# Kernel optimization log

Hardware: AMD Instinct MI355X
Metric: run time of the kernel (lower is better)

## Reference

```python
import jax, jax.numpy as jnp
import numpy as np

# Dims and constants
B, DIN, H = 32768, 256, 256
STEPS = 3                 # ode_steps (>1 -> RK2 branch)
DT = 1.0 / STEPS
TAU_MIN = 0.2
ALPHA = 0.1               # plastic (hebb) mixing coefficient
ETA = 0.1                 # hebb learning rate
DECAY = 0.99              # hebb trace decay
MOE_WEIGHT = 1.0


def setup_inputs() -> dict:
    key = jax.random.key(0)
    ks = jax.random.split(key, 8)
    s = 0.02
    return {
        "x": jax.random.normal(ks[0], (B, DIN), dtype=jnp.float32),
        "h": jax.random.normal(ks[1], (B, H), dtype=jnp.float32),
        "hebb_ih": jnp.zeros((DIN, H), dtype=jnp.float32),
        "hebb_hh": jnp.zeros((H, H), dtype=jnp.float32),
        # PlasticSynapse base weights (torch Linear layout [out, in])
        "W_ih": jax.random.normal(ks[2], (H, DIN), dtype=jnp.float32) * s,
        "b_ih": jnp.zeros((H,), dtype=jnp.float32),
        "W_hh": jax.random.normal(ks[3], (H, H), dtype=jnp.float32) * s,
        "b_hh": jnp.zeros((H,), dtype=jnp.float32),
        # tau_net: Linear(DIN+H -> H) -> SiLU -> Linear(H -> H) -> Softplus
        "W_t1": jax.random.normal(ks[4], (H, DIN + H), dtype=jnp.float32) * s,
        "b_t1": jnp.zeros((H,), dtype=jnp.float32),
        "W_t2": jax.random.normal(ks[5], (H, H), dtype=jnp.float32) * s,
        "b_t2": jnp.zeros((H,), dtype=jnp.float32),
    }


def reference(x, h, hebb_ih, hebb_hh, W_ih, b_ih, W_hh, b_hh, W_t1, b_t1, W_t2, b_t2):
    bsz = x.shape[0]
    step_moe = MOE_WEIGHT / STEPS

    def syn(inp, W, b, hebb):
        # PlasticSynapse: fixed weight + alpha-scaled Hebbian trace
        return inp @ (W.T + ALPHA * hebb) + b

    def tau_net(hh):
        z = jnp.concatenate([x, hh], axis=-1)          # [B, DIN+H]
        u = z @ W_t1.T + b_t1
        u = u * jax.nn.sigmoid(u)                      # SiLU
        return jax.nn.softplus(u @ W_t2.T + b_t2) + TAU_MIN

    def dynamics(hh, heb_ih, heb_hh):
        interaction = jnp.tanh(syn(x, W_ih, b_ih, heb_ih) + syn(hh, W_hh, b_hh, heb_hh))
        return (-hh + interaction) / tau_net(hh)

    def update_hebb(hebb, pre, post):
        # decayed trace + batch-mean outer product, scaled by per-step moe weight
        return DECAY * hebb + (ETA * step_moe / bsz) * (pre.T @ post)

    # RK2 loop (steps = 3, fixed) with mid-point Hebbian updates, per original forward
    for _ in range(STEPS):
        k1 = dynamics(h, hebb_ih, hebb_hh)
        h_mid = h + 0.5 * DT * k1
        hebb_ih = update_hebb(hebb_ih, x, h_mid)
        hebb_hh = update_hebb(hebb_hh, h_mid, h_mid)
        k2 = dynamics(h_mid, hebb_ih, hebb_hh)
        h = h + DT * k2
    return h
```

## Files before the change

### kernel.cpp

```cpp
#include <hip/hip_runtime.h>
#include <stdint.h>

typedef unsigned short u16;
typedef short v8s __attribute__((ext_vector_type(8)));
typedef short v4s __attribute__((ext_vector_type(4)));
typedef float v4f __attribute__((ext_vector_type(4)));

#define NB 32768
#define ND 256
#define DTF (1.0f/3.0f)
#define ALPHA 0.1f
#define DECAY 0.99f
#define TAU_MIN 0.2f
#define HEBB_SCALE (0.1f*(1.0f/3.0f)/32768.0f)

__device__ __forceinline__ float b2f(u16 h){ return __uint_as_float(((unsigned)h)<<16); }
__device__ __forceinline__ u16 f2b(float f){
  unsigned u = __float_as_uint(f);
  u += 0x7FFFu + ((u>>16)&1u);
  return (u16)(u>>16);
}

__device__ __forceinline__ void async16(const void* g, void* l){
  __builtin_amdgcn_global_load_lds((const __attribute__((address_space(1))) unsigned*)g,
                                   (__attribute__((address_space(3))) unsigned*)l, 16, 0, 0);
}

__device__ __forceinline__ void waitv(int n){
  switch(n){
    case 9: asm volatile("s_waitcnt vmcnt(9)" ::: "memory"); break;
    case 8: asm volatile("s_waitcnt vmcnt(8)" ::: "memory"); break;
    case 7: asm volatile("s_waitcnt vmcnt(7)" ::: "memory"); break;
    case 6: asm volatile("s_waitcnt vmcnt(6)" ::: "memory"); break;
    case 4: asm volatile("s_waitcnt vmcnt(4)" ::: "memory"); break;
    case 2: asm volatile("s_waitcnt vmcnt(2)" ::: "memory"); break;
    default: asm volatile("s_waitcnt vmcnt(0)" ::: "memory"); break;
  }
}

__global__ void k_copy(const float* __restrict__ x, const float* __restrict__ h,
                       u16* __restrict__ x_bf, u16* __restrict__ h_bf,
                       float* __restrict__ h_state){
  const long tot = (long)NB*ND/4;
  for (long i = blockIdx.x*(long)blockDim.x + threadIdx.x; i < tot;
       i += (long)gridDim.x*blockDim.x){
    v4f xv = *(const v4f*)(x + 4*i);
    v4f hv = *(const v4f*)(h + 4*i);
    u16 t4[4], t5[4];
#pragma unroll
    for (int e=0;e<4;++e){ t4[e] = f2b(xv[e]); t5[e] = f2b(hv[e]); }
    *(v4s*)(x_bf + 4*i) = *(v4s*)t4;
    *(v4s*)(h_bf + 4*i) = *(v4s*)t5;
    *(v4f*)(h_state + 4*i) = hv;
  }
}

__global__ void k_transpose_x(const float* __restrict__ x, u16* __restrict__ xT){
  __shared__ u16 ld[64*65];
  int bt = blockIdx.x >> 2, it = blockIdx.x & 3;
  long b0 = (long)bt*64; int i0 = it*64;
  int t = threadIdx.x;
#pragma unroll
  for (int e=0;e<16;++e){
    int idx = e*256 + t; int r = idx>>6, c = idx&63;
    ld[c + r*65] = f2b(x[(b0+r)*ND + i0 + c]);
  }
  __syncthreads();
#pragma unroll
  for (int e=0;e<16;++e){
    int idx = e*256 + t; int rr = idx>>6, cc = idx&63;
    xT[(long)(i0+rr)*NB + b0 + cc] = ld[cc*65 + rr];
  }
}

__global__ void k_prep_w(const float* __restrict__ W_ih, const float* __restrict__ W_hh,
                         const float* __restrict__ W_t1, const float* __restrict__ W_t2,
                         const float* __restrict__ hebb_ih, const float* __restrict__ hebb_hh,
                         u16* __restrict__ weff_ih, u16* __restrict__ weff_hh,
                         u16* __restrict__ wt1a, u16* __restrict__ wt1b, u16* __restrict__ wt2){
  int i = blockIdx.x*blockDim.x + threadIdx.x;
  if (i >= ND*ND) return;
  int n = i >> 8, k = i & 255;
  weff_ih[i] = f2b(W_ih[i] + ALPHA*hebb_ih[k*ND + n]);
  weff_hh[i] = f2b(W_hh[i] + ALPHA*hebb_hh[k*ND + n]);
  wt1a[i] = f2b(W_t1[n*512 + k]);
  wt1b[i] = f2b(W_t1[n*512 + 256 + k]);
  wt2[i]  = f2b(W_t2[i]);
}

__launch_bounds__(512,2)
__global__ void k_gemmP(const u16* __restrict__ x_bf, const u16* __restrict__ wt1a,
                        const float* __restrict__ b_t1, u16* __restrict__ P){
  __shared__ u16 lA[128*40];
  __shared__ u16 lB[256*40];
  int t = threadIdx.x, lid = t&63, wid = t>>6, wm = wid>>2, wn = wid&3, lr = lid&15, lg = lid>>4;
  long row0 = (long)blockIdx.x*128;
  v4f z = {0.f,0.f,0.f,0.f};
  v4f acc[4][4];
#pragma unroll
  for (int a=0;a<4;++a)
#pragma unroll
    for (int b=0;b<4;++b) acc[a][b] = z;
  for (int c=0; c<8; ++c){
    __syncthreads();
    { int r=t>>2, sg=t&3;
      *(v8s*)&lA[r*40+sg*8] = *(const v8s*)(x_bf + (row0+r)*ND + c*32 + sg*8); }
#pragma unroll
    for (int it2=0; it2<2; ++it2){
      int s2=t+it2*512; int n=s2>>2, sg=s2&3;
      *(v8s*)&lB[n*40+sg*8] = *(const v8s*)(wt1a + n*ND + c*32 + sg*8);
    }
    __syncthreads();
    v8s a[4], b[4];
#pragma unroll
    for (int mf=0;mf<4;++mf) a[mf] = *(v8s*)&lA[(wm*64+mf*16+lr)*40 + lg*8];
#pragma unroll
    for (int nf=0;nf<4;++nf) b[nf] = *(v8s*)&lB[(wn*64+nf*16+lr)*40 + lg*8];
#pragma unroll
    for (int mf=0;mf<4;++mf)
#pragma unroll
      for (int nf=0;nf<4;++nf)
        acc[mf][nf] = __builtin_amdgcn_mfma_f32_16x16x32_bf16(a[mf], b[nf], acc[mf][nf], 0,0,0);
  }
#pragma unroll
  for (int mf=0;mf<4;++mf)
#pragma unroll
    for (int nf=0;nf<4;++nf)
#pragma unroll
      for (int r=0;r<4;++r){
        int rr = wm*64+mf*16+lg*4+r, cc = wn*64+nf*16+lr;
        P[(row0+rr)*ND + cc] = f2b(acc[mf][nf][r] + b_t1[cc]);
      }
}

template<int BASEF, int WF, int WT>
__launch_bounds__(512,2)
__global__ void k_dyn2(const u16* __restrict__ x_bf, const u16* __restrict__ ev_bf,
                       const float* __restrict__ baseF,
                       const u16* __restrict__ weff_ih, const u16* __restrict__ weff_hh,
                       const u16* __restrict__ wt1b, const u16* __restrict__ wt2,
                       const u16* __restrict__ P,
                       const float* __restrict__ b_ih, const float* __restrict__ b_hh,
                       const float* __restrict__ b_t2, float coef,
                       float* __restrict__ outF, u16* __restrict__ outB, u16* __restrict__ outT){
  __shared__ u16 lA[5*64*32];
  __shared__ u16 lB[5*256*32];
  __shared__ u16 lU[64*296];
  __shared__ float sb1[256], sb2[256];
  const int t = threadIdx.x, lid = t&63, wid = t>>6;
  const int wm = wid>>2, wn = wid&3, lr = lid&15, lg = lid>>4;
  const long row0 = (long)blockIdx.x*64;

  if (t < 256){ sb1[t] = b_ih[t] + b_hh[t]; sb2[t] = b_t2[t]; }

  const int rA  = (wid&3)*16 + (lid>>2);
  const int scA = (lid&3) ^ ((rA>>1)&3);
  const long aoffg = (row0 + rA)*ND + scA*8;
  const int rB0 = wid*32 + (lid>>2), rB1 = rB0 + 16;
  const int boffg0 = rB0*ND + (((lid&3) ^ ((rB0>>1)&3))*8);
  const int boffg1 = rB1*ND + (((lid&3) ^ ((rB1>>1)&3))*8);

  int aoff[2], boff[4], uoffb[2];
#pragma unroll
  for (int mf=0;mf<2;++mf){
    int R = wm*32 + mf*16 + lr;
    aoff[mf] = R*32 + ((lg ^ ((R>>1)&3))*8);
    uoffb[mf] = R*296 + lg*8;
  }
#pragma unroll
  for (int nf=0;nf<4;++nf){
    int N = wn*64 + nf*16 + lr;
    boff[nf] = N*32 + ((lg ^ ((N>>1)&3))*8);
  }

  u16 Pv[32];
#pragma unroll
  for (int mf=0;mf<2;++mf)
#pragma unroll
    for (int nf=0;nf<4;++nf)
#pragma unroll
      for (int r=0;r<4;++r){
        int rr = wm*32+mf*16+lg*4+r, cc = wn*64+nf*16+lr;
        Pv[(mf*4+nf)*4+r] = P[(row0+rr)*ND + cc];
      }

  auto stageA = [&](int jj){
    if (wid < 4){
      const u16* src = (jj < 8) ? ev_bf : (jj < 16 ? x_bf : ev_bf);
      async16(src + aoffg + (jj&7)*32, lA + (jj%5)*2048 + (wid&3)*512);
    }
  };
  auto stageB = [&](int jj){
    const u16* W = (jj<8) ? wt1b : (jj<16 ? weff_ih : (jj<24 ? weff_hh : wt2));
    int c = (jj&7)*32;
    async16(W + c + boffg0, lB + (jj%5)*8192 + wid*1024);
    async16(W + c + boffg1, lB + (jj%5)*8192 + wid*1024 + 512);
  };

  stageB(0); stageA(0);
  stageB(1); stageA(1);
  stageB(2); stageA(2);
  stageB(3); stageA(3);
  __syncthreads();

  v4f z = {0.f,0.f,0.f,0.f};
  v4f acc2[2][4], accI[2][4], acc4[2][4];
#pragma unroll
  for (int a=0;a<2;++a)
#pragma unroll
    for (int b=0;b<4;++b){ acc2[a][b]=z; accI[a][b]=z; acc4[a][b]=z; }

#pragma unroll
  for (int j=0; j<32; ++j){
    int n;
    if (wid < 4) n = (j<=20)?9:((j==21)?8:((j==22)?7:((j<=28)?6:((j==29)?4:((j==30)?2:0)))));
    else         n = (j<=28)?6:((j==29)?4:((j==30)?2:0));
    waitv(n);
    __builtin_amdgcn_s_barrier();
    if (j <= 19) stageA(j+4);
    if (j <= 27) stageB(j+4);

    v8s b[4];
#pragma unroll
    for (int nf=0;nf<4;++nf) b[nf] = *(v8s*)&lB[(j%5)*8192 + boff[nf]];

    if (j < 24){
      v8s a[2];
#pragma unroll
      for (int mf=0;mf<2;++mf) a[mf] = *(v8s*)&lA[(j%5)*2048 + aoff[mf]];
      if (j < 8){
#pragma unroll
        for (int mf=0;mf<2;++mf)
#pragma unroll
          for (int nf=0;nf<4;++nf)
            acc2[mf][nf] = __builtin_amdgcn_mfma_f32_16x16x32_bf16(a[mf], b[nf], acc2[mf][nf], 0,0,0);
      } else {
#pragma unroll
        for (int mf=0;mf<2;++mf)
#pragma unroll
          for (int nf=0;nf<4;++nf)
            accI[mf][nf] = __builtin_amdgcn_mfma_f32_16x16x32_bf16(a[mf], b[nf], accI[mf][nf], 0,0,0);
      }
    } else {
      v8s a[2];
#pragma unroll
      for (int mf=0;mf<2;++mf) a[mf] = *(v8s*)&lU[uoffb[mf] + (j-24)*32];
#pragma unroll
      for (int mf=0;mf<2;++mf)
#pragma unroll
        for (int nf=0;nf<4;++nf)
          acc4[mf][nf] = __builtin_amdgcn_mfma_f32_16x16x32_bf16(a[mf], b[nf], acc4[mf][nf], 0,0,0);
    }

    if (j == 7){
#pragma unroll
      for (int mf=0;mf<2;++mf)
#pragma unroll
        for (int nf=0;nf<4;++nf)
#pragma unroll
          for (int r=0;r<4;++r){
            int rr = wm*32+mf*16+lg*4+r, cc = wn*64+nf*16+lr;
            float v = acc2[mf][nf][r] + b2f(Pv[(mf*4+nf)*4+r]);
            float sgm = 1.f/(1.f + __expf(-v));
            lU[rr*296 + cc] = f2b(v*sgm);
          }
      asm volatile("s_waitcnt lgkmcnt(0)" ::: "memory");
    }
  }

  __syncthreads();

#pragma unroll
  for (int mf=0;mf<2;++mf)
#pragma unroll
    for (int nf=0;nf<4;++nf)
#pragma unroll
      for (int r=0;r<4;++r){
        int rr = wm*32+mf*16+lg*4+r, cc = wn*64+nf*16+lr;
        long gi = (row0+rr)*ND + cc;
        float pre = accI[mf][nf][r] + sb1[cc];
        float pc = fminf(fmaxf(pre, -15.f), 15.f);
        float e2 = __expf(2.f*pc);
        float inter = (e2 - 1.f)/(e2 + 1.f);
        float zz = acc4[mf][nf][r] + sb2[cc];
        float sp = (zz > 15.f) ? zz : __logf(1.f + __expf(zz));
        float tau = sp + TAU_MIN;
        float bv, ev;
        if (BASEF){ bv = baseF[gi]; ev = b2f(ev_bf[gi]); }
        else      { bv = b2f(ev_bf[gi]); ev = bv; }
        float o = bv + coef*(inter - ev)/tau;
        if (WF) outF[gi] = o;
        outB[gi] = f2b(o);
        if (WT) lU[cc*72 + rr] = f2b(o);
      }
  if (WT){
    __syncthreads();
    int cc = t>>1, r0 = (t&1)*32;
#pragma unroll
    for (int e=0;e<4;++e){
      v8s v = *(v8s*)&lU[cc*72 + r0 + e*8];
      *(v8s*)(outT + (long)cc*NB + row0 + r0 + e*8) = v;
    }
  }
}

__launch_bounds__(512,2)
__global__ void k_hebb_part(const u16* __restrict__ xT, const u16* __restrict__ hmT,
                            u16* __restrict__ part){
  __shared__ u16 lA[256*40];
  __shared__ u16 lB[256*40];
  int t = threadIdx.x, lid = t&63, wid = t>>6, wm = wid>>2, wn = wid&3, lr = lid&15, lg = lid>>4;
  int mat = blockIdx.x & 1, chunk = blockIdx.x >> 1;
  const u16* Asrc = mat ? hmT : xT;
  v4f z = {0.f,0.f,0.f,0.f};
  v4f acc[8][4];
#pragma unroll
  for (int a=0;a<8;++a)
#pragma unroll
    for (int b=0;b<4;++b) acc[a][b] = z;
  for (int kc=0; kc<16; ++kc){
    long b0 = (long)chunk*512 + kc*32;
    __syncthreads();
#pragma unroll
    for (int it2=0; it2<2; ++it2){
      int s = t + it2*512; int rr = s>>2, sg = s&3;
      *(v8s*)&lA[rr*40+sg*8] = *(const v8s*)(Asrc + (long)rr*NB + b0 + sg*8);
      *(v8s*)&lB[rr*40+sg*8] = *(const v8s*)(hmT  + (long)rr*NB + b0 + sg*8);
    }
    __syncthreads();
    v8s a[8], b[4];
#pragma unroll
    for (int mf=0;mf<8;++mf) a[mf] = *(v8s*)&lA[(wm*128+mf*16+lr)*40 + lg*8];
#pragma unroll
    for (int nf=0;nf<4;++nf) b[nf] = *(v8s*)&lB[(wn*64+nf*16+lr)*40 + lg*8];
#pragma unroll
    for (int mf=0;mf<8;++mf)
#pragma unroll
      for (int nf=0;nf<4;++nf)
        acc[mf][nf] = __builtin_amdgcn_mfma_f32_16x16x32_bf16(a[mf], b[nf], acc[mf][nf], 0,0,0);
  }
  u16* dst = part + (long)blockIdx.x*65536;
#pragma unroll
  for (int mf=0;mf<8;++mf)
#pragma unroll
    for (int nf=0;nf<4;++nf)
#pragma unroll
      for (int r=0;r<4;++r){
        int i = wm*128+mf*16+lg*4+r, j = wn*64+nf*16+lr;
        dst[i*ND + j] = f2b(acc[mf][nf][r]);
      }
}

__global__ void k_hebb_reduce(const u16* __restrict__ part,
                              const float* __restrict__ prev_ih, const float* __restrict__ prev_hh,
                              float* __restrict__ next_ih, float* __restrict__ next_hh,
                              const float* __restrict__ W_ih, const float* __restrict__ W_hh,
                              u16* __restrict__ weff_ih, u16* __restrict__ weff_hh){
  int tid = blockIdx.x*blockDim.x + threadIdx.x;
  if (tid >= 2*ND*ND) return;
  int mat = tid >> 16;
  int rem = tid & 65535;
  float s = 0.f;
  for (int c=0; c<64; ++c) s += b2f(part[(long)((c<<1)+mat)*65536 + rem]);
  const float* prev = mat ? prev_hh : prev_ih;
  float nv = DECAY*prev[rem] + HEBB_SCALE*s;
  if (mat) next_hh[rem] = nv; else next_ih[rem] = nv;
  int k = rem >> 8, n = rem & 255;
  const float* Wb = mat ? W_hh : W_ih;
  u16 wv = f2b(Wb[n*ND + k] + ALPHA*nv);
  if (mat) weff_hh[n*ND + k] = wv; else weff_ih[n*ND + k] = wv;
}

extern "C" void kernel_launch(void* const* d_in, const int* in_sizes, int n_in,
                              void* d_out, int out_size, void* d_ws, size_t ws_size,
                              hipStream_t stream) {
  const float* x       = (const float*)d_in[0];
  const float* h       = (const float*)d_in[1];
  const float* hebb_ih = (const float*)d_in[2];
  const float* hebb_hh = (const float*)d_in[3];
  const float* W_ih    = (const float*)d_in[4];
  const float* b_ih    = (const float*)d_in[5];
  const float* W_hh    = (const float*)d_in[6];
  const float* b_hh    = (const float*)d_in[7];
  const float* W_t1    = (const float*)d_in[8];
  const float* b_t1    = (const float*)d_in[9];
  const float* W_t2    = (const float*)d_in[10];
  const float* b_t2    = (const float*)d_in[11];
  float* h_state = (float*)d_out;

  char* w = (char*)d_ws;
  u16* x_bf  = (u16*)w;  w += 16777216;
  u16* xT    = (u16*)w;  w += 16777216;
  u16* P     = (u16*)w;  w += 16777216;
  u16* hmT   = (u16*)w;  w += 16777216;
  u16* h_bf  = (u16*)w;  w += 16777216;
  u16* hm_bf = (u16*)w;  w += 16777216;
  u16* part  = (u16*)w;  w += 16777216;
  float* hebA_ih = (float*)w; w += 262144;
  float* hebA_hh = (float*)w; w += 262144;
  float* hebB_ih = (float*)w; w += 262144;
  float* hebB_hh = (float*)w; w += 262144;
  u16* weff_ih = (u16*)w; w += 131072;
  u16* weff_hh = (u16*)w; w += 131072;
  u16* wt1a    = (u16*)w; w += 131072;
  u16* wt1b    = (u16*)w; w += 131072;
  u16* wt2     = (u16*)w; w += 131072;
  if ((size_t)(w - (char*)d_ws) > ws_size) return;

  k_copy<<<2048,256,0,stream>>>(x, h, x_bf, h_bf, h_state);
  k_transpose_x<<<2048,256,0,stream>>>(x, xT);
  k_prep_w<<<256,256,0,stream>>>(W_ih,W_hh,W_t1,W_t2,hebb_ih,hebb_hh,
                                 weff_ih,weff_hh,wt1a,wt1b,wt2);
  k_gemmP<<<256,512,0,stream>>>(x_bf, wt1a, b_t1, P);

  const float* pih = hebb_ih; const float* phh = hebb_hh;
  for (int s=0; s<3; ++s){
    float* nih = (s&1) ? hebB_ih : hebA_ih;
    float* nhh = (s&1) ? hebB_hh : hebA_hh;
    k_dyn2<0,0,1><<<512,512,0,stream>>>(x_bf, h_bf, h_state, weff_ih, weff_hh, wt1b, wt2, P,
                                        b_ih, b_hh, b_t2, 0.5f*DTF,
                                        (float*)0, hm_bf, hmT);
    k_hebb_part<<<128,512,0,stream>>>(xT, hmT, part);
    k_hebb_reduce<<<512,256,0,stream>>>(part, pih, phh, nih, nhh, W_ih, W_hh, weff_ih, weff_hh);
    k_dyn2<1,1,0><<<512,512,0,stream>>>(x_bf, hm_bf, h_state, weff_ih, weff_hh, wt1b, wt2, P,
                                        b_ih, b_hh, b_t2, DTF,
                                        h_state, h_bf, (u16*)0);
    pih = nih; phh = nhh;
  }
}
```

Before: 711.6 us.

## Fuse init kernels, re-pipeline dyn and hebb GEMMs with async LDS staging

Merges the bf16 copy and x-transpose into one init kernel and drops the fp32 h_state copy by reading h directly in the first step. The dynamics kernel uses a unified 5-slot rolling async stage, a swizzled LDS layout for the SiLU intermediate, and setprio around MFMAs. On the last step it skips the bf16 output write. The Hebbian partial GEMM is rewritten with a 4-deep async global-to-LDS pipeline and twice as many blocks. This doubles the partial buffer and the number of partials the reduce kernel must sum.

```diff
diff --git a/kernel.cpp b/kernel.cpp
--- a/kernel.cpp
+++ b/kernel.cpp
@@ -28,49 +28,41 @@
 
 __device__ __forceinline__ void waitv(int n){
   switch(n){
-    case 9: asm volatile("s_waitcnt vmcnt(9)" ::: "memory"); break;
-    case 8: asm volatile("s_waitcnt vmcnt(8)" ::: "memory"); break;
-    case 7: asm volatile("s_waitcnt vmcnt(7)" ::: "memory"); break;
-    case 6: asm volatile("s_waitcnt vmcnt(6)" ::: "memory"); break;
-    case 4: asm volatile("s_waitcnt vmcnt(4)" ::: "memory"); break;
-    case 2: asm volatile("s_waitcnt vmcnt(2)" ::: "memory"); break;
-    default: asm volatile("s_waitcnt vmcnt(0)" ::: "memory"); break;
-  }
-}
-
-__global__ void k_copy(const float* __restrict__ x, const float* __restrict__ h,
+    case 12: asm volatile("s_waitcnt vmcnt(12)" ::: "memory"); break;
+    case 9:  asm volatile("s_waitcnt vmcnt(9)"  ::: "memory"); break;
+    case 8:  asm volatile("s_waitcnt vmcnt(8)"  ::: "memory"); break;
+    case 6:  asm volatile("s_waitcnt vmcnt(6)"  ::: "memory"); break;
+    case 4:  asm volatile("s_waitcnt vmcnt(4)"  ::: "memory"); break;
+    case 3:  asm volatile("s_waitcnt vmcnt(3)"  ::: "memory"); break;
+    case 2:  asm volatile("s_waitcnt vmcnt(2)"  ::: "memory"); break;
+    default: asm volatile("s_waitcnt vmcnt(0)"  ::: "memory"); break;
+  }
+}
+
+__global__ void k_init(const float* __restrict__ x, const float* __restrict__ h,
                        u16* __restrict__ x_bf, u16* __restrict__ h_bf,
-                       float* __restrict__ h_state){
-  const long tot = (long)NB*ND/4;
-  for (long i = blockIdx.x*(long)blockDim.x + threadIdx.x; i < tot;
-       i += (long)gridDim.x*blockDim.x){
-    v4f xv = *(const v4f*)(x + 4*i);
-    v4f hv = *(const v4f*)(h + 4*i);
-    u16 t4[4], t5[4];
-#pragma unroll
-    for (int e=0;e<4;++e){ t4[e] = f2b(xv[e]); t5[e] = f2b(hv[e]); }
-    *(v4s*)(x_bf + 4*i) = *(v4s*)t4;
-    *(v4s*)(h_bf + 4*i) = *(v4s*)t5;
-    *(v4f*)(h_state + 4*i) = hv;
-  }
-}
-
-__global__ void k_transpose_x(const float* __restrict__ x, u16* __restrict__ xT){
-  __shared__ u16 ld[64*65];
-  int bt = blockIdx.x >> 2, it = blockIdx.x & 3;
-  long b0 = (long)bt*64; int i0 = it*64;
-  int t = threadIdx.x;
-#pragma unroll
-  for (int e=0;e<16;++e){
-    int idx = e*256 + t; int r = idx>>6, c = idx&63;
-    ld[c + r*65] = f2b(x[(b0+r)*ND + i0 + c]);
+                       u16* __restrict__ xT){
+  __shared__ u16 lt[256*68];
+  const long r0 = (long)blockIdx.x*64;
+  const int t = threadIdx.x;
+#pragma unroll
+  for (int e=0; e<16; ++e){
+    int i = e*1024 + t*4;
+    int row = i>>8, col = i&255;
+    v4f xv = *(const v4f*)(x + (r0+row)*ND + col);
+    v4f hv = *(const v4f*)(h + (r0+row)*ND + col);
+    u16 a4[4], b4[4];
+#pragma unroll
+    for (int k=0;k<4;++k){ a4[k]=f2b(xv[k]); b4[k]=f2b(hv[k]); }
+    *(v4s*)(x_bf + (r0+row)*ND + col) = *(v4s*)a4;
+    *(v4s*)(h_bf + (r0+row)*ND + col) = *(v4s*)b4;
+#pragma unroll
+    for (int k=0;k<4;++k) lt[(col+k)*68 + row] = a4[k];
   }
   __syncthreads();
 #pragma unroll
-  for (int e=0;e<16;++e){
-    int idx = e*256 + t; int rr = idx>>6, cc = idx&63;
-    xT[(long)(i0+rr)*NB + b0 + cc] = ld[cc*65 + rr];
-  }
+  for (int e=0; e<16; ++e)
+    *(v4s*)(xT + (long)t*NB + r0 + e*4) = *(v4s*)&lt[t*68 + e*4];
 }
 
 __global__ void k_prep_w(const float* __restrict__ W_ih, const float* __restrict__ W_hh,
@@ -133,9 +125,9 @@
       }
 }
 
-template<int BASEF, int WF, int WT>
+template<int BASEF, int WF, int WT, int WB>
 __launch_bounds__(512,2)
-__global__ void k_dyn2(const u16* __restrict__ x_bf, const u16* __restrict__ ev_bf,
+__global__ void k_dyn3(const u16* __restrict__ x_bf, const u16* __restrict__ ev_bf,
                        const float* __restrict__ baseF,
                        const u16* __restrict__ weff_ih, const u16* __restrict__ weff_hh,
                        const u16* __restrict__ wt1b, const u16* __restrict__ wt2,
@@ -143,9 +135,9 @@
                        const float* __restrict__ b_ih, const float* __restrict__ b_hh,
                        const float* __restrict__ b_t2, float coef,
                        float* __restrict__ outF, u16* __restrict__ outB, u16* __restrict__ outT){
-  __shared__ u16 lA[5*64*32];
-  __shared__ u16 lB[5*256*32];
-  __shared__ u16 lU[64*296];
+  __shared__ u16 lA[5*2048];
+  __shared__ u16 lB[5*8192];
+  __shared__ u16 lU[64*272];
   __shared__ float sb1[256], sb2[256];
   const int t = threadIdx.x, lid = t&63, wid = t>>6;
   const int wm = wid>>2, wn = wid&3, lr = lid&15, lg = lid>>4;
@@ -154,18 +146,17 @@
   if (t < 256){ sb1[t] = b_ih[t] + b_hh[t]; sb2[t] = b_t2[t]; }
 
   const int rA  = (wid&3)*16 + (lid>>2);
-  const int scA = (lid&3) ^ ((rA>>1)&3);
-  const long aoffg = (row0 + rA)*ND + scA*8;
+  const long aoffg = (row0 + rA)*ND + (((lid&3) ^ ((rA>>1)&3))*8);
   const int rB0 = wid*32 + (lid>>2), rB1 = rB0 + 16;
   const int boffg0 = rB0*ND + (((lid&3) ^ ((rB0>>1)&3))*8);
   const int boffg1 = rB1*ND + (((lid&3) ^ ((rB1>>1)&3))*8);
 
-  int aoff[2], boff[4], uoffb[2];
+  int aoff[2], boff[4], uoff[2];
 #pragma unroll
   for (int mf=0;mf<2;++mf){
     int R = wm*32 + mf*16 + lr;
     aoff[mf] = R*32 + ((lg ^ ((R>>1)&3))*8);
-    uoffb[mf] = R*296 + lg*8;
+    uoff[mf] = R*272 + ((lg ^ ((R>>1)&3))*8);
   }
 #pragma unroll
   for (int nf=0;nf<4;++nf){
@@ -173,6 +164,16 @@
     boff[nf] = N*32 + ((lg ^ ((N>>1)&3))*8);
   }
 
+  auto stage = [&](int jj, int sl){
+    const u16* asrc = (jj<8) ? ev_bf : (jj<16 ? x_bf : (jj<24 ? ev_bf : x_bf));
+    const u16* W    = (jj<8) ? wt1b  : (jj<16 ? weff_ih : (jj<24 ? weff_hh : wt2));
+    const int c = (jj&7)*32;
+    if (wid < 4) async16(asrc + aoffg + c, lA + sl*2048 + (wid&3)*512);
+    async16(W + c + boffg0, lB + sl*8192 + wid*1024);
+    async16(W + c + boffg1, lB + sl*8192 + wid*1024 + 512);
+  };
+
+  stage(0,0); stage(1,1); stage(2,2); stage(3,3);
   u16 Pv[32];
 #pragma unroll
   for (int mf=0;mf<2;++mf)
@@ -183,24 +184,6 @@
         int rr = wm*32+mf*16+lg*4+r, cc = wn*64+nf*16+lr;
         Pv[(mf*4+nf)*4+r] = P[(row0+rr)*ND + cc];
       }
-
-  auto stageA = [&](int jj){
-    if (wid < 4){
-      const u16* src = (jj < 8) ? ev_bf : (jj < 16 ? x_bf : ev_bf);
-      async16(src + aoffg + (jj&7)*32, lA + (jj%5)*2048 + (wid&3)*512);
-    }
-  };
-  auto stageB = [&](int jj){
-    const u16* W = (jj<8) ? wt1b : (jj<16 ? weff_ih : (jj<24 ? weff_hh : wt2));
-    int c = (jj&7)*32;
-    async16(W + c + boffg0, lB + (jj%5)*8192 + wid*1024);
-    async16(W + c + boffg1, lB + (jj%5)*8192 + wid*1024 + 512);
-  };
-
-  stageB(0); stageA(0);
-  stageB(1); stageA(1);
-  stageB(2); stageA(2);
-  stageB(3); stageA(3);
   __syncthreads();
 
   v4f z = {0.f,0.f,0.f,0.f};
@@ -210,47 +193,46 @@
 #pragma unroll
     for (int b=0;b<4;++b){ acc2[a][b]=z; accI[a][b]=z; acc4[a][b]=z; }
 
-#pragma unroll
+  int rs = 0, wsl = 4;
   for (int j=0; j<32; ++j){
-    int n;
-    if (wid < 4) n = (j<=20)?9:((j==21)?8:((j==22)?7:((j<=28)?6:((j==29)?4:((j==30)?2:0)))));
-    else         n = (j<=28)?6:((j==29)?4:((j==30)?2:0));
-    waitv(n);
+    int m3 = 31-j; if (m3 > 3) m3 = 3;
+    waitv(m3 * (wid<4 ? 3 : 2));
     __builtin_amdgcn_s_barrier();
-    if (j <= 19) stageA(j+4);
-    if (j <= 27) stageB(j+4);
+    if (j <= 27) stage(j+4, wsl);
 
     v8s b[4];
 #pragma unroll
-    for (int nf=0;nf<4;++nf) b[nf] = *(v8s*)&lB[(j%5)*8192 + boff[nf]];
-
+    for (int nf=0;nf<4;++nf) b[nf] = *(v8s*)&lB[rs*8192 + boff[nf]];
+    v8s a[2];
     if (j < 24){
-      v8s a[2];
-#pragma unroll
-      for (int mf=0;mf<2;++mf) a[mf] = *(v8s*)&lA[(j%5)*2048 + aoff[mf]];
-      if (j < 8){
-#pragma unroll
-        for (int mf=0;mf<2;++mf)
-#pragma unroll
-          for (int nf=0;nf<4;++nf)
-            acc2[mf][nf] = __builtin_amdgcn_mfma_f32_16x16x32_bf16(a[mf], b[nf], acc2[mf][nf], 0,0,0);
-      } else {
-#pragma unroll
-        for (int mf=0;mf<2;++mf)
-#pragma unroll
-          for (int nf=0;nf<4;++nf)
-            accI[mf][nf] = __builtin_amdgcn_mfma_f32_16x16x32_bf16(a[mf], b[nf], accI[mf][nf], 0,0,0);
-      }
+#pragma unroll
+      for (int mf=0;mf<2;++mf) a[mf] = *(v8s*)&lA[rs*2048 + aoff[mf]];
     } else {
-      v8s a[2];
-#pragma unroll
-      for (int mf=0;mf<2;++mf) a[mf] = *(v8s*)&lU[uoffb[mf] + (j-24)*32];
+#pragma unroll
+      for (int mf=0;mf<2;++mf) a[mf] = *(v8s*)&lU[uoff[mf] + (j&7)*32];
+    }
+
+    __builtin_amdgcn_s_setprio(1);
+    if (j < 8){
+#pragma unroll
+      for (int mf=0;mf<2;++mf)
+#pragma unroll
+        for (int nf=0;nf<4;++nf)
+          acc2[mf][nf] = __builtin_amdgcn_mfma_f32_16x16x32_bf16(a[mf], b[nf], acc2[mf][nf], 0,0,0);
+    } else if (j < 24){
+#pragma unroll
+      for (int mf=0;mf<2;++mf)
+#pragma unroll
+        for (int nf=0;nf<4;++nf)
+          accI[mf][nf] = __builtin_amdgcn_mfma_f32_16x16x32_bf16(a[mf], b[nf], accI[mf][nf], 0,0,0);
+    } else {
 #pragma unroll
       for (int mf=0;mf<2;++mf)
 #pragma unroll
         for (int nf=0;nf<4;++nf)
           acc4[mf][nf] = __builtin_amdgcn_mfma_f32_16x16x32_bf16(a[mf], b[nf], acc4[mf][nf], 0,0,0);
     }
+    __builtin_amdgcn_s_setprio(0);
 
     if (j == 7){
 #pragma unroll
@@ -262,10 +244,12 @@
             int rr = wm*32+mf*16+lg*4+r, cc = wn*64+nf*16+lr;
             float v = acc2[mf][nf][r] + b2f(Pv[(mf*4+nf)*4+r]);
             float sgm = 1.f/(1.f + __expf(-v));
-            lU[rr*296 + cc] = f2b(v*sgm);
+            int w = cc>>5, ch = (cc>>3)&3;
+            lU[rr*272 + w*32 + ((ch ^ ((rr>>1)&3))*8) + (cc&7)] = f2b(v*sgm);
           }
       asm volatile("s_waitcnt lgkmcnt(0)" ::: "memory");
     }
+    rs = (rs==4)?0:rs+1; wsl = (wsl==4)?0:wsl+1;
   }
 
   __syncthreads();
@@ -290,55 +274,83 @@
         else      { bv = b2f(ev_bf[gi]); ev = bv; }
         float o = bv + coef*(inter - ev)/tau;
         if (WF) outF[gi] = o;
-        outB[gi] = f2b(o);
-        if (WT) lU[cc*72 + rr] = f2b(o);
+        if (WB) outB[gi] = f2b(o);
+        if (WT) lU[cc*68 + rr] = f2b(o);
       }
   if (WT){
     __syncthreads();
-    int cc = t>>1, r0 = (t&1)*32;
-#pragma unroll
-    for (int e=0;e<4;++e){
-      v8s v = *(v8s*)&lU[cc*72 + r0 + e*8];
-      *(v8s*)(outT + (long)cc*NB + row0 + r0 + e*8) = v;
-    }
+    int cc = t>>1, r0b = (t&1)*32;
+#pragma unroll
+    for (int e=0;e<8;++e)
+      *(v4s*)(outT + (long)cc*NB + row0 + r0b + e*4) = *(v4s*)&lU[cc*68 + r0b + e*4];
   }
 }
 
 __launch_bounds__(512,2)
-__global__ void k_hebb_part(const u16* __restrict__ xT, const u16* __restrict__ hmT,
-                            u16* __restrict__ part){
-  __shared__ u16 lA[256*40];
-  __shared__ u16 lB[256*40];
-  int t = threadIdx.x, lid = t&63, wid = t>>6, wm = wid>>2, wn = wid&3, lr = lid&15, lg = lid>>4;
-  int mat = blockIdx.x & 1, chunk = blockIdx.x >> 1;
+__global__ void k_hebb_part2(const u16* __restrict__ xT, const u16* __restrict__ hmT,
+                             u16* __restrict__ part){
+  __shared__ u16 lA[4*8192];
+  __shared__ u16 lB[4*8192];
+  const int t = threadIdx.x, lid = t&63, wid = t>>6;
+  const int wm = wid>>2, wn = wid&3, lr = lid&15, lg = lid>>4;
+  const int mat = blockIdx.x & 1, chunk = blockIdx.x >> 1;
   const u16* Asrc = mat ? hmT : xT;
+  const long col0 = (long)chunk*256;
+
+  const int r0s = wid*32 + (lid>>2), r1s = r0s + 16;
+  const long goff0 = (long)r0s*NB + (((lid&3) ^ ((r0s>>1)&3))*8);
+  const long goff1 = (long)r1s*NB + (((lid&3) ^ ((r1s>>1)&3))*8);
+
+  int aoff[8], boff[4];
+#pragma unroll
+  for (int mf=0;mf<8;++mf){
+    int R = wm*128 + mf*16 + lr;
+    aoff[mf] = R*32 + ((lg ^ ((R>>1)&3))*8);
+  }
+#pragma unroll
+  for (int nf=0;nf<4;++nf){
+    int N = wn*64 + nf*16 + lr;
+    boff[nf] = N*32 + ((lg ^ ((N>>1)&3))*8);
+  }
+
+  auto stage = [&](int kc, int sl){
+    const long c = col0 + kc*32;
+    async16(Asrc + goff0 + c, lA + sl*8192 + wid*1024);
+    async16(Asrc + goff1 + c, lA + sl*8192 + wid*1024 + 512);
+    async16(hmT  + goff0 + c, lB + sl*8192 + wid*1024);
+    async16(hmT  + goff1 + c, lB + sl*8192 + wid*1024 + 512);
+  };
+
+  stage(0,0); stage(1,1); stage(2,2);
+  __syncthreads();
+
   v4f z = {0.f,0.f,0.f,0.f};
   v4f acc[8][4];
 #pragma unroll
   for (int a=0;a<8;++a)
 #pragma unroll
     for (int b=0;b<4;++b) acc[a][b] = z;
-  for (int kc=0; kc<16; ++kc){
-    long b0 = (long)chunk*512 + kc*32;
-    __syncthreads();
-#pragma unroll
-    for (int it2=0; it2<2; ++it2){
-      int s = t + it2*512; int rr = s>>2, sg = s&3;
-      *(v8s*)&lA[rr*40+sg*8] = *(const v8s*)(Asrc + (long)rr*NB + b0 + sg*8);
-      *(v8s*)&lB[rr*40+sg*8] = *(const v8s*)(hmT  + (long)rr*NB + b0 + sg*8);
-    }
-    __syncthreads();
+
+  for (int j=0; j<8; ++j){
+    int m2 = 7-j; if (m2 > 2) m2 = 2;
+    waitv(m2*4);
+    __builtin_amdgcn_s_barrier();
+    if (j <= 4) stage(j+3, (j+3)&3);
+    const int rs = j&3;
     v8s a[8], b[4];
 #pragma unroll
-    for (int mf=0;mf<8;++mf) a[mf] = *(v8s*)&lA[(wm*128+mf*16+lr)*40 + lg*8];
-#pragma unroll
-    for (int nf=0;nf<4;++nf) b[nf] = *(v8s*)&lB[(wn*64+nf*16+lr)*40 + lg*8];
+    for (int mf=0;mf<8;++mf) a[mf] = *(v8s*)&lA[rs*8192 + aoff[mf]];
+#pragma unroll
+    for (int nf=0;nf<4;++nf) b[nf] = *(v8s*)&lB[rs*8192 + boff[nf]];
+    __builtin_amdgcn_s_setprio(1);
 #pragma unroll
     for (int mf=0;mf<8;++mf)
 #pragma unroll
       for (int nf=0;nf<4;++nf)
         acc[mf][nf] = __builtin_amdgcn_mfma_f32_16x16x32_bf16(a[mf], b[nf], acc[mf][nf], 0,0,0);
-  }
+    __builtin_amdgcn_s_setprio(0);
+  }
+
   u16* dst = part + (long)blockIdx.x*65536;
 #pragma unroll
   for (int mf=0;mf<8;++mf)
@@ -346,8 +358,8 @@
     for (int nf=0;nf<4;++nf)
 #pragma unroll
       for (int r=0;r<4;++r){
-        int i = wm*128+mf*16+lg*4+r, j = wn*64+nf*16+lr;
-        dst[i*ND + j] = f2b(acc[mf][nf][r]);
+        int i = wm*128+mf*16+lg*4+r, jj = wn*64+nf*16+lr;
+        dst[i*ND + jj] = f2b(acc[mf][nf][r]);
       }
 }
 
@@ -361,7 +373,7 @@
   int mat = tid >> 16;
   int rem = tid & 65535;
   float s = 0.f;
-  for (int c=0; c<64; ++c) s += b2f(part[(long)((c<<1)+mat)*65536 + rem]);
+  for (int c=0; c<128; ++c) s += b2f(part[(long)((c<<1)+mat)*65536 + rem]);
   const float* prev = mat ? prev_hh : prev_ih;
   float nv = DECAY*prev[rem] + HEBB_SCALE*s;
   if (mat) next_hh[rem] = nv; else next_ih[rem] = nv;
@@ -395,7 +407,7 @@
   u16* hmT   = (u16*)w;  w += 16777216;
   u16* h_bf  = (u16*)w;  w += 16777216;
   u16* hm_bf = (u16*)w;  w += 16777216;
-  u16* part  = (u16*)w;  w += 16777216;
+  u16* part  = (u16*)w;  w += 33554432;
   float* hebA_ih = (float*)w; w += 262144;
   float* hebA_hh = (float*)w; w += 262144;
   float* hebB_ih = (float*)w; w += 262144;
@@ -407,8 +419,7 @@
   u16* wt2     = (u16*)w; w += 131072;
   if ((size_t)(w - (char*)d_ws) > ws_size) return;
 
-  k_copy<<<2048,256,0,stream>>>(x, h, x_bf, h_bf, h_state);
-  k_transpose_x<<<2048,256,0,stream>>>(x, xT);
+  k_init<<<512,256,0,stream>>>(x, h, x_bf, h_bf, xT);
   k_prep_w<<<256,256,0,stream>>>(W_ih,W_hh,W_t1,W_t2,hebb_ih,hebb_hh,
                                  weff_ih,weff_hh,wt1a,wt1b,wt2);
   k_gemmP<<<256,512,0,stream>>>(x_bf, wt1a, b_t1, P);
@@ -417,14 +428,23 @@
   for (int s=0; s<3; ++s){
     float* nih = (s&1) ? hebB_ih : hebA_ih;
     float* nhh = (s&1) ? hebB_hh : hebA_hh;
-    k_dyn2<0,0,1><<<512,512,0,stream>>>(x_bf, h_bf, h_state, weff_ih, weff_hh, wt1b, wt2, P,
-                                        b_ih, b_hh, b_t2, 0.5f*DTF,
-                                        (float*)0, hm_bf, hmT);
-    k_hebb_part<<<128,512,0,stream>>>(xT, hmT, part);
+    k_dyn3<0,0,1,1><<<512,512,0,stream>>>(x_bf, h_bf, (const float*)0,
+                                          weff_ih, weff_hh, wt1b, wt2, P,
+                                          b_ih, b_hh, b_t2, 0.5f*DTF,
+                                          (float*)0, hm_bf, hmT);
+    k_hebb_part2<<<256,512,0,stream>>>(xT, hmT, part);
     k_hebb_reduce<<<512,256,0,stream>>>(part, pih, phh, nih, nhh, W_ih, W_hh, weff_ih, weff_hh);
-    k_dyn2<1,1,0><<<512,512,0,stream>>>(x_bf, hm_bf, h_state, weff_ih, weff_hh, wt1b, wt2, P,
-                                        b_ih, b_hh, b_t2, DTF,
-                                        h_state, h_bf, (u16*)0);
+    const float* base = (s==0) ? h : (const float*)h_state;
+    if (s < 2)
+      k_dyn3<1,1,0,1><<<512,512,0,stream>>>(x_bf, hm_bf, base,
+                                            weff_ih, weff_hh, wt1b, wt2, P,
+                                            b_ih, b_hh, b_t2, DTF,
+                                            h_state, h_bf, (u16*)0);
+    else
+      k_dyn3<1,1,0,0><<<512,512,0,stream>>>(x_bf, hm_bf, base,
+                                            weff_ih, weff_hh, wt1b, wt2, P,
+                                            b_ih, b_hh, b_t2, DTF,
+                                            h_state, (u16*)0, (u16*)0);
     pih = nih; phh = nhh;
   }
 }
```

Measured after the change: 1.112 ms. 1.56x slower.
